# Performance work log

Measured on AMD Instinct MI355X. Metric: run time of the kernel, lower is better.

Reference implementation:

```python
import jax, jax.numpy as jnp
import numpy as np

B, N, D_IN, D_OUT = 4, 2048, 1024, 1024

def setup_inputs() -> dict:
    key = jax.random.key(0)
    ks = jax.random.split(key, 7)
    s_in = 1.0 / np.sqrt(D_IN)
    return {
        "X": jax.random.normal(ks[0], (B, N, D_IN), dtype=jnp.float32),
        "Wq": jax.random.uniform(ks[1], (D_IN, D_OUT), jnp.float32, -s_in, s_in),
        "bq": jax.random.uniform(ks[2], (D_OUT,), jnp.float32, -s_in, s_in),
        "Wk": jax.random.uniform(ks[3], (D_IN, D_OUT), jnp.float32, -s_in, s_in),
        "bk": jax.random.uniform(ks[4], (D_OUT,), jnp.float32, -s_in, s_in),
        "Wv": jax.random.uniform(ks[5], (D_IN, D_OUT), jnp.float32, -s_in, s_in),
        "bv": jax.random.uniform(ks[6], (D_OUT,), jnp.float32, -s_in, s_in),
    }

def reference(X, Wq, bq, Wk, bk, Wv, bv):
    # QKV projections: [B,N,D_in] @ [D_in,D_out] -> [B,N,D_out]
    q = jnp.einsum('bnd,de->bne', X, Wq) + bq
    k = jnp.einsum('bnd,de->bne', X, Wk) + bk
    v = jnp.einsum('bnd,de->bne', X, Wv) + bv
    # Unscaled attention (faithful: original has no 1/sqrt(d))
    scores = jnp.einsum('bne,bme->bnm', q, k)  # [B,N,N]
    weights = jax.nn.softmax(scores, axis=-1)
    return jnp.einsum('bnm,bme->bne', weights, v)
```

## Files before the change

kernel.cpp:

```cpp
#include <hip/hip_runtime.h>
#include <hip/hip_bf16.h>
#include <hip/hip_fp16.h>
#include <stdint.h>
#include <math.h>


typedef unsigned short ushort_t;
typedef __attribute__((ext_vector_type(8))) _Float16  f16x8;
typedef __attribute__((ext_vector_type(4))) _Float16  f16x4;
typedef __attribute__((ext_vector_type(4))) float     f32x4;

__device__ __forceinline__ void async_load16(const void* g, void* l) {
  __builtin_amdgcn_global_load_lds(
      (const __attribute__((address_space(1))) void*)g,
      (__attribute__((address_space(3))) void*)l, 16, 0, 0);
}

#define BARR do { __builtin_amdgcn_sched_barrier(0); \
                  __builtin_amdgcn_s_barrier();      \
                  __builtin_amdgcn_sched_barrier(0); } while (0)

#define NA0 0
#define NB0 16384
#define NA1 24576
#define NB1 40960

__device__ __forceinline__ void stage_A_n(const ushort_t* __restrict__ gb, long ldk,
                                          int k0, int q, ushort_t* lt, int t)
{
#pragma unroll
  for (int j = 0; j < 2; ++j) {
    const int i   = j * 64 + (t >> 3);
    const int row = ((i >> 5) << 6) | (q << 5) | (i & 31);
    const int ch  = (t & 7) ^ (row & 7);
    async_load16(gb + (long)row * ldk + k0 + ch * 8, lt + row * 64 + (t & 7) * 8);
  }
}

__device__ __forceinline__ void stage_B_n(const ushort_t* __restrict__ gb, long ldk,
                                          int k0, int q, ushort_t* lt, int t)
{
  const int i   = t >> 3;
  const int row = ((i >> 5) << 6) | (q << 5) | (i & 31);
  const int ch  = (t & 7) ^ (row & 7);
  async_load16(gb + (long)row * ldk + k0 + ch * 8, lt + row * 64 + (t & 7) * 8);
}

#define RD_A4(SET, BASE, QM)                                                  \
  do { _Pragma("unroll") for (int m_ = 0; m_ < 2; ++m_) {                     \
    SET[m_][0] = *(const f16x8*)&lds[(BASE) + (arow_l + (QM)*32 + m_*16) * 64 + ck0]; \
    SET[m_][1] = *(const f16x8*)&lds[(BASE) + (arow_l + (QM)*32 + m_*16) * 64 + ck1]; \
  } } while (0)

#define RD_B4(SET, BASE)                                                      \
  do { _Pragma("unroll") for (int q_ = 0; q_ < 2; ++q_)                       \
    _Pragma("unroll") for (int n_ = 0; n_ < 2; ++n_) {                        \
      SET[q_][n_][0] = *(const f16x8*)&lds[(BASE) + (brow_l + q_*32 + n_*16) * 64 + ck0]; \
      SET[q_][n_][1] = *(const f16x8*)&lds[(BASE) + (brow_l + q_*32 + n_*16) * 64 + ck1]; \
    } } while (0)

#define MM16(AS, BS, QM)                                                      \
  do { __builtin_amdgcn_s_setprio(1);                                         \
  _Pragma("unroll") for (int kh_ = 0; kh_ < 2; ++kh_)                         \
    _Pragma("unroll") for (int m_ = 0; m_ < 2; ++m_)                          \
      _Pragma("unroll") for (int n_ = 0; n_ < 2; ++n_) {                      \
        acc[(QM)*2+m_][n_]   = __builtin_amdgcn_mfma_f32_16x16x32_f16(        \
            AS[m_][kh_], BS[0][n_][kh_], acc[(QM)*2+m_][n_], 0, 0, 0);        \
        acc[(QM)*2+m_][2+n_] = __builtin_amdgcn_mfma_f32_16x16x32_f16(        \
            AS[m_][kh_], BS[1][n_][kh_], acc[(QM)*2+m_][2+n_], 0, 0, 0);      \
      }                                                                       \
  __builtin_amdgcn_s_setprio(0); } while (0)

#define MM16S(AS, BS, QM, SC)                                                 \
  do { __builtin_amdgcn_s_setprio(1);                                         \
  _Pragma("unroll") for (int m_ = 0; m_ < 2; ++m_)                            \
    _Pragma("unroll") for (int kh_ = 0; kh_ < 2; ++kh_) {                     \
      const f16x8 as_ = AS[m_][kh_] * (_Float16)(SC)[(QM)*2+m_];              \
      _Pragma("unroll") for (int n_ = 0; n_ < 2; ++n_) {                      \
        acc[(QM)*2+m_][n_]   = __builtin_amdgcn_mfma_f32_16x16x32_f16(        \
            as_, BS[0][n_][kh_], acc[(QM)*2+m_][n_], 0, 0, 0);                \
        acc[(QM)*2+m_][2+n_] = __builtin_amdgcn_mfma_f32_16x16x32_f16(        \
            as_, BS[1][n_][kh_], acc[(QM)*2+m_][2+n_], 0, 0, 0);              \
      } }                                                                     \
  __builtin_amdgcn_s_setprio(0); } while (0)

template<bool LAST>
__device__ __forceinline__ void iterRA(const ushort_t* __restrict__ Ab,
                                       const ushort_t* __restrict__ Bb,
                                       long lda, long ldb,
                                       ushort_t* lds, f32x4 (&acc)[4][4],
                                       int ka, int t, int arow_l, int brow_l,
                                       int ck0, int ck1,
                                       f16x8 (&aF)[2][2], f16x8 (&aG)[2][2],
                                       f16x8 (&bF)[2][2][2], f16x8 (&bG)[2][2][2])
{
  const int kc = ka + 128, kd = ka + 192;

  RD_A4(aG, NA0, 1);
  if constexpr (!LAST) { stage_A_n(Ab, lda, kc, 0, lds + NA0, t);
                         stage_B_n(Bb, ldb, kc, 0, lds + NB0, t); }
  BARR;
  MM16(aF, bF, 0);
  if constexpr (LAST) asm volatile("s_waitcnt vmcnt(0)" ::: "memory");
  else                asm volatile("s_waitcnt vmcnt(3)" ::: "memory");
  BARR;
  RD_A4(aF, NA1, 0);
  RD_B4(bG, NB1);
  if constexpr (!LAST) { stage_A_n(Ab, lda, kc, 1, lds + NA0, t);
                         stage_B_n(Bb, ldb, kc, 1, lds + NB0, t); }
  BARR;
  MM16(aG, bF, 1);
  BARR;
  RD_A4(aG, NA1, 1);
  if constexpr (!LAST) { stage_A_n(Ab, lda, kd, 0, lds + NA1, t);
                         stage_B_n(Bb, ldb, kd, 0, lds + NB1, t); }
  BARR;
  MM16(aF, bG, 0);
  if constexpr (!LAST) asm volatile("s_waitcnt vmcnt(3)" ::: "memory");
  BARR;
  if constexpr (!LAST) {
    RD_A4(aF, NA0, 0);
    RD_B4(bF, NB0);
    stage_A_n(Ab, lda, kd, 1, lds + NA1, t);
    stage_B_n(Bb, ldb, kd, 1, lds + NB1, t);
  }
  BARR;
  MM16(aG, bG, 1);
  BARR;
}

template<bool LAST>
__device__ __forceinline__ void pv_iterRA(const ushort_t* __restrict__ Ab,
                                          const ushort_t* __restrict__ Bb,
                                          ushort_t* lds, const float (*ScL)[256],
                                          f32x4 (&acc)[4][4],
                                          int ka, int t, int arow_l, int brow_l,
                                          int ck0, int ck1,
                                          f16x8 (&aF)[2][2], f16x8 (&aG)[2][2],
                                          f16x8 (&bF)[2][2][2], f16x8 (&bG)[2][2][2])
{
  const int kc = ka + 128, kd = ka + 192;
  const int cba = ka >> 6;
  float sa4[4], sb4[4];
#pragma unroll
  for (int s = 0; s < 4; ++s) {
    sa4[s] = ScL[cba][arow_l + s * 16];
    sb4[s] = ScL[cba + 1][arow_l + s * 16];
  }

  RD_A4(aG, NA0, 1);
  if constexpr (!LAST) { stage_A_n(Ab, 2048, kc, 0, lds + NA0, t);
                         stage_B_n(Bb, 2048, kc, 0, lds + NB0, t); }
  BARR;
  MM16S(aF, bF, 0, sa4);
  if constexpr (LAST) asm volatile("s_waitcnt vmcnt(0)" ::: "memory");
  else                asm volatile("s_waitcnt vmcnt(3)" ::: "memory");
  BARR;
  RD_A4(aF, NA1, 0);
  RD_B4(bG, NB1);
  if constexpr (!LAST) { stage_A_n(Ab, 2048, kc, 1, lds + NA0, t);
                         stage_B_n(Bb, 2048, kc, 1, lds + NB0, t); }
  BARR;
  MM16S(aG, bF, 1, sa4);
  BARR;
  RD_A4(aG, NA1, 1);
  if constexpr (!LAST) { stage_A_n(Ab, 2048, kd, 0, lds + NA1, t);
                         stage_B_n(Bb, 2048, kd, 0, lds + NB1, t); }
  BARR;
  MM16S(aF, bG, 0, sb4);
  if constexpr (!LAST) asm volatile("s_waitcnt vmcnt(3)" ::: "memory");
  BARR;
  if constexpr (!LAST) {
    RD_A4(aF, NA0, 0);
    RD_B4(bF, NB0);
    stage_A_n(Ab, 2048, kd, 1, lds + NA1, t);
    stage_B_n(Bb, 2048, kd, 1, lds + NB1, t);
  }
  BARR;
  MM16S(aG, bG, 1, sb4);
  BARR;
}

#define PROLOGUE_RA(LDA, LDB)                               \
  do {                                                      \
    stage_A_n(Ab, (LDA),  0, 0, lds + NA0, t);              \
    stage_B_n(Bb, (LDB),  0, 0, lds + NB0, t);              \
    stage_A_n(Ab, (LDA),  0, 1, lds + NA0, t);              \
    stage_B_n(Bb, (LDB),  0, 1, lds + NB0, t);              \
    asm volatile("s_waitcnt vmcnt(0)" ::: "memory");        \
    BARR;                                                   \
    RD_A4(aF, NA0, 0);                                      \
    RD_B4(bF, NB0);                                         \
    stage_A_n(Ab, (LDA), 64, 0, lds + NA1, t);              \
    stage_B_n(Bb, (LDB), 64, 0, lds + NB1, t);              \
    stage_A_n(Ab, (LDA), 64, 1, lds + NA1, t);              \
    stage_B_n(Bb, (LDB), 64, 1, lds + NB1, t);              \
    BARR;                                                   \
  } while (0)

__global__ __launch_bounds__(512, 2)
void qkv_ra_kernel(const ushort_t* __restrict__ A, const ushort_t* __restrict__ BT,
                   const float* __restrict__ bq, const float* __restrict__ bk,
                   const float* __restrict__ bvp,
                   __half* __restrict__ Qh, __half* __restrict__ Kh,
                   ushort_t* __restrict__ Vt)
{
  __shared__ __align__(16) ushort_t lds[49152];

  const int nb = gridDim.x * gridDim.y;
  int id = blockIdx.y * gridDim.x + blockIdx.x;
  id = (id & 7) * (nb >> 3) + (id >> 3);
  const int bx = id % gridDim.x;
  const int by = id / gridDim.x;

  const ushort_t* Ab = A  + (long)by * 256 * 1024;
  const ushort_t* Bb = BT + (long)bx * 128 * 1024;

  const int t    = threadIdx.x;
  const int lane = t & 63;
  const int wave = t >> 6;
  const int wr   = wave >> 1;
  const int wc   = wave & 1;
  const int arow_l = wr * 64 + (lane & 15);
  const int brow_l = wc * 64 + (lane & 15);
  const int ck0 = (((lane >> 4)    ) ^ (lane & 7)) * 8;
  const int ck1 = ((4 + (lane >> 4)) ^ (lane & 7)) * 8;

  f32x4 acc[4][4];
  const f32x4 zero = {0.0f, 0.0f, 0.0f, 0.0f};
#pragma unroll
  for (int i = 0; i < 4; ++i)
#pragma unroll
    for (int j = 0; j < 4; ++j) acc[i][j] = zero;

  f16x8 aF[2][2], aG[2][2], bF[2][2][2], bG[2][2][2];

  PROLOGUE_RA(1024, 1024);
#pragma unroll 1
  for (int it = 0; it < 7; ++it)
    iterRA<false>(Ab, Bb, 1024, 1024, lds, acc, it * 128, t, arow_l, brow_l,
                  ck0, ck1, aF, aG, bF, bG);
  iterRA<true>(Ab, Bb, 1024, 1024, lds, acc, 896, t, arow_l, brow_l,
               ck0, ck1, aF, aG, bF, bG);

  const int er = (lane >> 4) * 4, ec = lane & 15;
  const int tgt = bx >> 3;
  const float* bias = (tgt == 0) ? bq : (tgt == 1) ? bk : bvp;

#pragma unroll
  for (int ni = 0; ni < 4; ++ni) {
    const int col = (bx & 7) * 128 + wc * 64 + ni * 16 + ec;
    const float bval = bias[col];
#pragma unroll
    for (int mi = 0; mi < 4; ++mi) {
      const long grow0 = (long)by * 256 + wr * 64 + mi * 16 + er;
      if (tgt < 2) {
        __half* o = (tgt == 0) ? Qh : Kh;
#pragma unroll
        for (int r = 0; r < 4; ++r)
          o[(grow0 + r) * 1024 + col] = __float2half(acc[mi][ni][r] + bval);
      } else {
        const long b  = grow0 >> 11;
        const long ml = grow0 & 2047;
        f16x4 v4;
#pragma unroll
        for (int r = 0; r < 4; ++r) v4[r] = (_Float16)(acc[mi][ni][r] + bval);
        *(f16x4*)&Vt[b * 2097152 + (long)col * 2048 + ml] = v4;
      }
    }
  }
}

__global__ __launch_bounds__(512, 2)
void qk_ra_kernel(const ushort_t* __restrict__ Q, const ushort_t* __restrict__ Kh,
                  __half* __restrict__ S, float* __restrict__ PM, float* __restrict__ PS)
{
  __shared__ __align__(16) ushort_t lds[49152];

  const int nb = gridDim.x * gridDim.y;
  int id = blockIdx.y * gridDim.x + blockIdx.x;
  id = (id & 7) * (nb >> 3) + (id >> 3);
  const int bx = id % gridDim.x;
  const int by = id / gridDim.x;
  const long z = blockIdx.z;

  const ushort_t* Ab = Q  + z * 2048 * 1024 + (long)by * 256 * 1024;
  const ushort_t* Bb = Kh + z * 2048 * 1024 + (long)bx * 128 * 1024;
  __half* Sb = S + z * 2048 * 2048;

  const int t    = threadIdx.x;
  const int lane = t & 63;
  const int wave = t >> 6;
  const int wr   = wave >> 1;
  const int wc   = wave & 1;
  const int arow_l = wr * 64 + (lane & 15);
  const int brow_l = wc * 64 + (lane & 15);
  const int ck0 = (((lane >> 4)    ) ^ (lane & 7)) * 8;
  const int ck1 = ((4 + (lane >> 4)) ^ (lane & 7)) * 8;

  f32x4 acc[4][4];
  const f32x4 zero = {0.0f, 0.0f, 0.0f, 0.0f};
#pragma unroll
  for (int i = 0; i < 4; ++i)
#pragma unroll
    for (int j = 0; j < 4; ++j) acc[i][j] = zero;

  f16x8 aF[2][2], aG[2][2], bF[2][2][2], bG[2][2][2];

  PROLOGUE_RA(1024, 1024);
#pragma unroll 1
  for (int it = 0; it < 7; ++it)
    iterRA<false>(Ab, Bb, 1024, 1024, lds, acc, it * 128, t, arow_l, brow_l,
                  ck0, ck1, aF, aG, bF, bG);
  iterRA<true>(Ab, Bb, 1024, 1024, lds, acc, 896, t, arow_l, brow_l,
               ck0, ck1, aF, aG, bF, bG);

  const int er = (lane >> 4) * 4, ec = lane & 15;
  const int cc = bx * 2 + wc;
  float* PMb = PM + z * 32 * 2048 + (long)cc * 2048;
  float* PSb = PS + z * 32 * 2048 + (long)cc * 2048;

#pragma unroll
  for (int mi = 0; mi < 4; ++mi)
#pragma unroll
    for (int r = 0; r < 4; ++r) {
      float m = fmaxf(fmaxf(acc[mi][0][r], acc[mi][1][r]),
                      fmaxf(acc[mi][2][r], acc[mi][3][r]));
      m = fmaxf(m, __shfl_xor(m, 1));
      m = fmaxf(m, __shfl_xor(m, 2));
      m = fmaxf(m, __shfl_xor(m, 4));
      m = fmaxf(m, __shfl_xor(m, 8));
      float s = 0.0f;
#pragma unroll
      for (int ni = 0; ni < 4; ++ni) {
        const float e = __expf(acc[mi][ni][r] - m);
        acc[mi][ni][r] = e;
        s += e;
      }
      s += __shfl_xor(s, 1);
      s += __shfl_xor(s, 2);
      s += __shfl_xor(s, 4);
      s += __shfl_xor(s, 8);
      if (ec == 0) {
        const long row = (long)by * 256 + wr * 64 + mi * 16 + er + r;
        PMb[row] = m;
        PSb[row] = s;
      }
    }

#pragma unroll
  for (int ni = 0; ni < 4; ++ni) {
    const long col = (long)bx * 128 + wc * 64 + ni * 16 + ec;
#pragma unroll
    for (int mi = 0; mi < 4; ++mi)
#pragma unroll
      for (int r = 0; r < 4; ++r) {
        const long grow = (long)by * 256 + wr * 64 + mi * 16 + er + r;
        Sb[grow * 2048 + col] = __float2half(acc[mi][ni][r]);
      }
  }
}

__global__ __launch_bounds__(512, 2)
void pv_ra_kernel(const ushort_t* __restrict__ S, const ushort_t* __restrict__ Vt,
                  const float* __restrict__ PM, const float* __restrict__ PS,
                  float* __restrict__ Out)
{
  __shared__ __align__(16) ushort_t lds[49152];
  __shared__ float ScL[32][256];

  const int nb = gridDim.x * gridDim.y;
  int id = blockIdx.y * gridDim.x + blockIdx.x;
  id = (id & 7) * (nb >> 3) + (id >> 3);
  const int bx = id % gridDim.x;
  const int by = id / gridDim.x;
  const long z = blockIdx.z;

  const ushort_t* Ab = S  + z * 4194304 + (long)by * 256 * 2048;
  const ushort_t* Bb = Vt + z * 2097152 + (long)bx * 128 * 2048;
  float* Cb = Out + z * 2048 * 1024;

  const int t = threadIdx.x;

  if (t < 256) {
    const long row = (long)by * 256 + t;
    const float* PMb = PM + z * 32 * 2048;
    const float* PSb = PS + z * 32 * 2048;
    float pm[32];
    float m = -3.4e38f;
#pragma unroll
    for (int cb = 0; cb < 32; ++cb) {
      pm[cb] = PMb[(long)cb * 2048 + row];
      m = fmaxf(m, pm[cb]);
    }
    float l = 0.0f;
#pragma unroll
    for (int cb = 0; cb < 32; ++cb)
      l += PSb[(long)cb * 2048 + row] * __expf(pm[cb] - m);
    const float inv = 1.0f / l;
#pragma unroll
    for (int cb = 0; cb < 32; ++cb)
      ScL[cb][t] = __expf(pm[cb] - m) * inv;
  }
  __syncthreads();

  const int lane = t & 63;
  const int wave = t >> 6;
  const int wr   = wave >> 1;
  const int wc   = wave & 1;
  const int arow_l = wr * 64 + (lane & 15);
  const int brow_l = wc * 64 + (lane & 15);
  const int ck0 = (((lane >> 4)    ) ^ (lane & 7)) * 8;
  const int ck1 = ((4 + (lane >> 4)) ^ (lane & 7)) * 8;

  f32x4 acc[4][4];
  const f32x4 zero = {0.0f, 0.0f, 0.0f, 0.0f};
#pragma unroll
  for (int i = 0; i < 4; ++i)
#pragma unroll
    for (int j = 0; j < 4; ++j) acc[i][j] = zero;

  f16x8 aF[2][2], aG[2][2], bF[2][2][2], bG[2][2][2];

  PROLOGUE_RA(2048, 2048);
#pragma unroll 1
  for (int it = 0; it < 15; ++it)
    pv_iterRA<false>(Ab, Bb, lds, ScL, acc, it * 128, t, arow_l, brow_l,
                     ck0, ck1, aF, aG, bF, bG);
  pv_iterRA<true>(Ab, Bb, lds, ScL, acc, 1920, t, arow_l, brow_l,
                  ck0, ck1, aF, aG, bF, bG);

  const int er = (lane >> 4) * 4, ec = lane & 15;
#pragma unroll
  for (int ni = 0; ni < 4; ++ni) {
    const int gcol = bx * 128 + wc * 64 + ni * 16 + ec;
#pragma unroll
    for (int mi = 0; mi < 4; ++mi) {
#pragma unroll
      for (int r = 0; r < 4; ++r) {
        const long grow = (long)by * 256 + wr * 64 + mi * 16 + er + r;
        Cb[grow * 1024 + gcol] = acc[mi][ni][r];
      }
    }
  }
}

__global__ __launch_bounds__(256)
void prep_kernel(const float* __restrict__ W0, const float* __restrict__ W1,
                 const float* __restrict__ W2, __half* __restrict__ dstW,
                 const float* __restrict__ X, __half* __restrict__ Xh)
{
  __shared__ float tile[32][33];
  const int z = blockIdx.z;
  if (z < 3) {
    const float* src = (z == 0) ? W0 : (z == 1) ? W1 : W2;
    __half* d = dstW + (long)z * 1024 * 1024;
    const int c0 = blockIdx.x * 32;
    const int r0 = blockIdx.y * 32;
    const int tx = threadIdx.x & 31;
    const int ty = threadIdx.x >> 5;
#pragma unroll
    for (int i = 0; i < 32; i += 8)
      tile[ty + i][tx] = src[(long)(r0 + ty + i) * 1024 + (c0 + tx)];
    __syncthreads();
#pragma unroll
    for (int i = 0; i < 32; i += 8)
      d[(long)(c0 + ty + i) * 1024 + (r0 + tx)] = __float2half(tile[tx][ty + i]);
  } else {
    const int bid = blockIdx.y * gridDim.x + blockIdx.x;
    const long i = (((long)(z - 3) * 1024 + bid) * 256 + threadIdx.x) * 8;
    const float4 a = *(const float4*)(X + i);
    const float4 b = *(const float4*)(X + i + 4);
    f16x8 h;
    h[0] = (_Float16)a.x; h[1] = (_Float16)a.y; h[2] = (_Float16)a.z; h[3] = (_Float16)a.w;
    h[4] = (_Float16)b.x; h[5] = (_Float16)b.y; h[6] = (_Float16)b.z; h[7] = (_Float16)b.w;
    *(f16x8*)((ushort_t*)Xh + i) = h;
  }
}

__global__ __launch_bounds__(256)
void cvt_f32_f16_kernel(const float* __restrict__ src, __half* __restrict__ dst, long n)
{
  const long i = ((long)blockIdx.x * 256 + threadIdx.x) * 8;
  if (i + 8 > n) return;
  const float4 a = *(const float4*)(src + i);
  const float4 b = *(const float4*)(src + i + 4);
  f16x8 h;
  h[0] = (_Float16)a.x; h[1] = (_Float16)a.y; h[2] = (_Float16)a.z; h[3] = (_Float16)a.w;
  h[4] = (_Float16)b.x; h[5] = (_Float16)b.y; h[6] = (_Float16)b.z; h[7] = (_Float16)b.w;
  *(f16x8*)((ushort_t*)dst + i) = h;
}

__global__ __launch_bounds__(256)
void transpose_cvt3_kernel(const float* __restrict__ W0, const float* __restrict__ W1,
                           const float* __restrict__ W2, __half* __restrict__ dst)
{
  __shared__ float tile[32][33];
  const int z = blockIdx.z;
  const float* src = (z == 0) ? W0 : (z == 1) ? W1 : W2;
  __half* d = dst + (long)z * 1024 * 1024;
  const int c0 = blockIdx.x * 32;
  const int r0 = blockIdx.y * 32;
  const int tx = threadIdx.x & 31;
  const int ty = threadIdx.x >> 5;
#pragma unroll
  for (int i = 0; i < 32; i += 8)
    tile[ty + i][tx] = src[(long)(r0 + ty + i) * 1024 + (c0 + tx)];
  __syncthreads();
#pragma unroll
  for (int i = 0; i < 32; i += 8)
    d[(long)(c0 + ty + i) * 1024 + (r0 + tx)] = __float2half(tile[tx][ty + i]);
}

extern "C" void kernel_launch(void* const* d_in, const int* in_sizes, int n_in,
                              void* d_out, int out_size, void* d_ws, size_t ws_size,
                              hipStream_t stream)
{
  const int  Bb = 4, Nn = 2048, Dd = 1024;
  const long BN = (long)Bb * Nn;

  const float* X  = (const float*)d_in[0];
  const float* Wq = (const float*)d_in[1];
  const float* bq = (const float*)d_in[2];
  const float* Wk = (const float*)d_in[3];
  const float* bk = (const float*)d_in[4];
  const float* Wv = (const float*)d_in[5];
  const float* bv = (const float*)d_in[6];
  float* Out      = (float*)d_out;

  uint8_t* w = (uint8_t*)d_ws;
  ushort_t* Wt = (ushort_t*)w;  w += (size_t)3 * Dd * Dd * 2;

  const size_t statsBytes = (size_t)Bb * 32 * Nn * 4;
  const size_t fullNeed = (size_t)3 * Dd * Dd * 2
                        + 4 * ((size_t)BN * Dd * 2)
                        + (size_t)Bb * Nn * Nn * 2
                        + 2 * statsBytes;

  if (ws_size >= fullNeed) {
    ushort_t* Xh = (ushort_t*)w;  w += (size_t)BN * Dd * 2;
    ushort_t* Q  = (ushort_t*)w;  w += (size_t)BN * Dd * 2;
    ushort_t* Kb = (ushort_t*)w;  w += (size_t)BN * Dd * 2;
    ushort_t* Vt = (ushort_t*)w;  w += (size_t)BN * Dd * 2;
    ushort_t* S  = (ushort_t*)w;  w += (size_t)Bb * Nn * Nn * 2;
    float*    PM = (float*)w;     w += statsBytes;
    float*    PS = (float*)w;

    prep_kernel<<<dim3(32, 32, 7), 256, 0, stream>>>(Wq, Wk, Wv, (__half*)Wt, X, (__half*)Xh);

    qkv_ra_kernel<<<dim3(3 * Dd / 128, BN / 256, 1), 512, 0, stream>>>(
        Xh, Wt, bq, bk, bv, (__half*)Q, (__half*)Kb, Vt);

    qk_ra_kernel<<<dim3(Nn / 128, Nn / 256, Bb), 512, 0, stream>>>(
        Q, Kb, (__half*)S, PM, PS);

    pv_ra_kernel<<<dim3(Dd / 128, Nn / 256, Bb), 512, 0, stream>>>(
        S, Vt, PM, PS, Out);
  } else {
    ushort_t* Xh = (ushort_t*)w;  w += (size_t)Nn * Dd * 2;
    ushort_t* Q  = (ushort_t*)w;  w += (size_t)Nn * Dd * 2;
    ushort_t* Kb = (ushort_t*)w;  w += (size_t)Nn * Dd * 2;
    ushort_t* Vt = (ushort_t*)w;  w += (size_t)Nn * Dd * 2;
    ushort_t* S  = (ushort_t*)w;  w += (size_t)Nn * Nn * 2;
    float*    PM = (float*)w;     w += (size_t)32 * Nn * 4;
    float*    PS = (float*)w;

    transpose_cvt3_kernel<<<dim3(Dd / 32, Dd / 32, 3), 256, 0, stream>>>(Wq, Wk, Wv, (__half*)Wt);

    for (int b = 0; b < Bb; ++b) {
      const float* Xb = X + (long)b * Nn * Dd;
      cvt_f32_f16_kernel<<<dim3((unsigned)((long)Nn * Dd / (8 * 256))), 256, 0, stream>>>(
          Xb, (__half*)Xh, (long)Nn * Dd);
      qkv_ra_kernel<<<dim3(3 * Dd / 128, Nn / 256, 1), 512, 0, stream>>>(
          Xh, Wt, bq, bk, bv, (__half*)Q, (__half*)Kb, Vt);
      qk_ra_kernel<<<dim3(Nn / 128, Nn / 256, 1), 512, 0, stream>>>(
          Q, Kb, (__half*)S, PM, PS);
      pv_ra_kernel<<<dim3(Dd / 128, Nn / 256, 1), 512, 0, stream>>>(
          S, Vt, PM, PS, Out + (long)b * Nn * Dd);
    }
  }
}
```

Baseline: 245.3 us.

## Use 256x256 output tiles for Q/K projection and QK^T GEMMs

Adds a new GEMM pipeline (iterQ) with 256x256 block tiles, where each wave computes 128x64 with eight by four accumulators. The QK^T scores kernel and a new Q/K projection kernel use it, and the V projection (transposed output) moves to its own kernel with the old 256x128 tile. Larger tiles raise arithmetic intensity and cut global and LDS traffic per FLOP. In exchange they double accumulator registers and use 128KB of LDS per block, which may hurt occupancy, and the QK grid shrinks to 256 blocks. The fallback path is rewired to reuse prep_kernel.

```diff
diff --git a/kernel.cpp b/kernel.cpp
--- a/kernel.cpp
+++ b/kernel.cpp
@@ -20,13 +20,8 @@
                   __builtin_amdgcn_s_barrier();      \
                   __builtin_amdgcn_sched_barrier(0); } while (0)
 
-#define NA0 0
-#define NB0 16384
-#define NA1 24576
-#define NB1 40960
-
-__device__ __forceinline__ void stage_A_n(const ushort_t* __restrict__ gb, long ldk,
-                                          int k0, int q, ushort_t* lt, int t)
+__device__ __forceinline__ void stage_h256(const ushort_t* __restrict__ gb, long ldk,
+                                           int k0, int q, ushort_t* lt, int t)
 {
 #pragma unroll
   for (int j = 0; j < 2; ++j) {
@@ -37,14 +32,136 @@
   }
 }
 
-__device__ __forceinline__ void stage_B_n(const ushort_t* __restrict__ gb, long ldk,
-                                          int k0, int q, ushort_t* lt, int t)
+__device__ __forceinline__ void stage_h128(const ushort_t* __restrict__ gb, long ldk,
+                                           int k0, int q, ushort_t* lt, int t)
 {
   const int i   = t >> 3;
   const int row = ((i >> 5) << 6) | (q << 5) | (i & 31);
   const int ch  = (t & 7) ^ (row & 7);
   async_load16(gb + (long)row * ldk + k0 + ch * 8, lt + row * 64 + (t & 7) * 8);
 }
+
+#define QA0 0
+#define QB0 16384
+#define QA1 32768
+#define QB1 49152
+
+#define RD_AG(SET, BASE, G)                                                   \
+  do { _Pragma("unroll") for (int mi_ = 0; mi_ < 4; ++mi_) {                  \
+    const int r_ = arow_l + (2*(G) + (mi_ & 1) + 4*(mi_ >> 1)) * 16;          \
+    SET[mi_][0] = *(const f16x8*)&lds[(BASE) + r_ * 64 + ck0];                \
+    SET[mi_][1] = *(const f16x8*)&lds[(BASE) + r_ * 64 + ck1];                \
+  } } while (0)
+
+#define RD_BH(SET, BASE, H)                                                   \
+  do { _Pragma("unroll") for (int ni_ = 0; ni_ < 2; ++ni_) {                  \
+    const int r_ = brow_l + (2*(H) + ni_) * 16;                               \
+    SET[ni_][0] = *(const f16x8*)&lds[(BASE) + r_ * 64 + ck0];                \
+    SET[ni_][1] = *(const f16x8*)&lds[(BASE) + r_ * 64 + ck1];                \
+  } } while (0)
+
+#define MM16G(AS, BS, G, H)                                                   \
+  do { __builtin_amdgcn_s_setprio(1);                                         \
+  _Pragma("unroll") for (int kh_ = 0; kh_ < 2; ++kh_)                         \
+    _Pragma("unroll") for (int mi_ = 0; mi_ < 4; ++mi_)                       \
+      _Pragma("unroll") for (int ni_ = 0; ni_ < 2; ++ni_)                     \
+        acc[2*(G) + (mi_ & 1) + 4*(mi_ >> 1)][2*(H) + ni_] =                  \
+            __builtin_amdgcn_mfma_f32_16x16x32_f16(                           \
+                AS[mi_][kh_], BS[ni_][kh_],                                   \
+                acc[2*(G) + (mi_ & 1) + 4*(mi_ >> 1)][2*(H) + ni_], 0, 0, 0); \
+  __builtin_amdgcn_s_setprio(0); } while (0)
+
+template<bool LAST>
+__device__ __forceinline__ void iterQ(const ushort_t* __restrict__ Ab,
+                                      const ushort_t* __restrict__ Bb,
+                                      long lda, long ldb,
+                                      ushort_t* lds, f32x4 (&acc)[8][4],
+                                      int ka, int t, int arow_l, int brow_l,
+                                      int ck0, int ck1,
+                                      f16x8 (&aF)[4][2], f16x8 (&aG)[4][2],
+                                      f16x8 (&bF)[2][2], f16x8 (&bG)[2][2])
+{
+  const int kc = ka + 128, kd = ka + 192;
+
+  RD_BH(bG, QB0, 1);
+  if constexpr (!LAST) stage_h256(Bb, ldb, kc, 0, lds + QB0, t);
+  BARR; MM16G(aF, bF, 0, 0); BARR;
+
+  RD_AG(aG, QA0, 1);
+  if constexpr (!LAST) stage_h256(Bb, ldb, kc, 1, lds + QB0, t);
+  BARR; MM16G(aF, bG, 0, 1);
+  if constexpr (LAST) asm volatile("s_waitcnt vmcnt(2)" ::: "memory");
+  else                asm volatile("s_waitcnt vmcnt(6)" ::: "memory");
+  BARR;
+
+  RD_AG(aF, QA1, 0);
+  if constexpr (!LAST) stage_h256(Ab, lda, kc, 0, lds + QA0, t);
+  BARR; MM16G(aG, bG, 1, 1); BARR;
+
+  RD_BH(bG, QB1, 0);
+  if constexpr (!LAST) stage_h256(Ab, lda, kc, 1, lds + QA0, t);
+  BARR; MM16G(aG, bF, 1, 0); BARR;
+
+  RD_BH(bF, QB1, 1);
+  if constexpr (!LAST) stage_h256(Bb, ldb, kd, 0, lds + QB1, t);
+  BARR; MM16G(aF, bG, 0, 0);
+  if constexpr (LAST) asm volatile("s_waitcnt vmcnt(0)" ::: "memory");
+  else                asm volatile("s_waitcnt vmcnt(10)" ::: "memory");
+  BARR;
+
+  RD_AG(aG, QA1, 1);
+  if constexpr (!LAST) stage_h256(Bb, ldb, kd, 1, lds + QB1, t);
+  BARR; MM16G(aF, bF, 0, 1);
+  if constexpr (!LAST) asm volatile("s_waitcnt vmcnt(6)" ::: "memory");
+  BARR;
+
+  if constexpr (!LAST) {
+    RD_AG(aF, QA0, 0);
+    stage_h256(Ab, lda, kd, 0, lds + QA1, t);
+  }
+  BARR; MM16G(aG, bF, 1, 1); BARR;
+
+  if constexpr (!LAST) {
+    RD_BH(bF, QB0, 0);
+    stage_h256(Ab, lda, kd, 1, lds + QA1, t);
+  }
+  BARR; MM16G(aG, bG, 1, 0);
+  if constexpr (!LAST) asm volatile("s_waitcnt vmcnt(8)" ::: "memory");
+  BARR;
+}
+
+#define PROLOGUE_Q(LDA, LDB)                                \
+  do {                                                      \
+    stage_h256(Bb, (LDB),  0, 0, lds + QB0, t);             \
+    stage_h256(Bb, (LDB),  0, 1, lds + QB0, t);             \
+    stage_h256(Ab, (LDA),  0, 0, lds + QA0, t);             \
+    stage_h256(Ab, (LDA),  0, 1, lds + QA0, t);             \
+    stage_h256(Bb, (LDB), 64, 0, lds + QB1, t);             \
+    stage_h256(Bb, (LDB), 64, 1, lds + QB1, t);             \
+    stage_h256(Ab, (LDA), 64, 0, lds + QA1, t);             \
+    stage_h256(Ab, (LDA), 64, 1, lds + QA1, t);             \
+    asm volatile("s_waitcnt vmcnt(8)" ::: "memory");        \
+    BARR;                                                   \
+    RD_AG(aF, QA0, 0);                                      \
+    RD_BH(bF, QB0, 0);                                      \
+    BARR;                                                   \
+  } while (0)
+
+#define GEMM_Q(LDA, LDB)                                                      \
+  do {                                                                        \
+    PROLOGUE_Q(LDA, LDB);                                                     \
+    _Pragma("unroll 1")                                                       \
+    for (int it = 0; it < 7; ++it)                                            \
+      iterQ<false>(Ab, Bb, (LDA), (LDB), lds, acc, it * 128, t,               \
+                   arow_l, brow_l, ck0, ck1, aF, aG, bF, bG);                 \
+    iterQ<true>(Ab, Bb, (LDA), (LDB), lds, acc, 896, t,                       \
+                arow_l, brow_l, ck0, ck1, aF, aG, bF, bG);                    \
+  } while (0)
+
+#define NA0 0
+#define NB0 16384
+#define NA1 24576
+#define NB1 40960
 
 #define RD_A4(SET, BASE, QM)                                                  \
   do { _Pragma("unroll") for (int m_ = 0; m_ < 2; ++m_) {                     \
@@ -97,32 +214,35 @@
   const int kc = ka + 128, kd = ka + 192;
 
   RD_A4(aG, NA0, 1);
-  if constexpr (!LAST) { stage_A_n(Ab, lda, kc, 0, lds + NA0, t);
-                         stage_B_n(Bb, ldb, kc, 0, lds + NB0, t); }
+  if constexpr (!LAST) { stage_h256(Ab, lda, kc, 0, lds + NA0, t);
+                         stage_h128(Bb, ldb, kc, 0, lds + NB0, t); }
   BARR;
   MM16(aF, bF, 0);
   if constexpr (LAST) asm volatile("s_waitcnt vmcnt(0)" ::: "memory");
   else                asm volatile("s_waitcnt vmcnt(3)" ::: "memory");
   BARR;
+
   RD_A4(aF, NA1, 0);
   RD_B4(bG, NB1);
-  if constexpr (!LAST) { stage_A_n(Ab, lda, kc, 1, lds + NA0, t);
-                         stage_B_n(Bb, ldb, kc, 1, lds + NB0, t); }
+  if constexpr (!LAST) { stage_h256(Ab, lda, kc, 1, lds + NA0, t);
+                         stage_h128(Bb, ldb, kc, 1, lds + NB0, t); }
   BARR;
   MM16(aG, bF, 1);
   BARR;
+
   RD_A4(aG, NA1, 1);
-  if constexpr (!LAST) { stage_A_n(Ab, lda, kd, 0, lds + NA1, t);
-                         stage_B_n(Bb, ldb, kd, 0, lds + NB1, t); }
+  if constexpr (!LAST) { stage_h256(Ab, lda, kd, 0, lds + NA1, t);
+                         stage_h128(Bb, ldb, kd, 0, lds + NB1, t); }
   BARR;
   MM16(aF, bG, 0);
   if constexpr (!LAST) asm volatile("s_waitcnt vmcnt(3)" ::: "memory");
   BARR;
+
   if constexpr (!LAST) {
     RD_A4(aF, NA0, 0);
     RD_B4(bF, NB0);
-    stage_A_n(Ab, lda, kd, 1, lds + NA1, t);
-    stage_B_n(Bb, ldb, kd, 1, lds + NB1, t);
+    stage_h256(Ab, lda, kd, 1, lds + NA1, t);
+    stage_h128(Bb, ldb, kd, 1, lds + NB1, t);
   }
   BARR;
   MM16(aG, bG, 1);
@@ -149,32 +269,35 @@
   }
 
   RD_A4(aG, NA0, 1);
-  if constexpr (!LAST) { stage_A_n(Ab, 2048, kc, 0, lds + NA0, t);
-                         stage_B_n(Bb, 2048, kc, 0, lds + NB0, t); }
+  if constexpr (!LAST) { stage_h256(Ab, 2048, kc, 0, lds + NA0, t);
+                         stage_h128(Bb, 2048, kc, 0, lds + NB0, t); }
   BARR;
   MM16S(aF, bF, 0, sa4);
   if constexpr (LAST) asm volatile("s_waitcnt vmcnt(0)" ::: "memory");
   else                asm volatile("s_waitcnt vmcnt(3)" ::: "memory");
   BARR;
+
   RD_A4(aF, NA1, 0);
   RD_B4(bG, NB1);
-  if constexpr (!LAST) { stage_A_n(Ab, 2048, kc, 1, lds + NA0, t);
-                         stage_B_n(Bb, 2048, kc, 1, lds + NB0, t); }
+  if constexpr (!LAST) { stage_h256(Ab, 2048, kc, 1, lds + NA0, t);
+                         stage_h128(Bb, 2048, kc, 1, lds + NB0, t); }
   BARR;
   MM16S(aG, bF, 1, sa4);
   BARR;
+
   RD_A4(aG, NA1, 1);
-  if constexpr (!LAST) { stage_A_n(Ab, 2048, kd, 0, lds + NA1, t);
-                         stage_B_n(Bb, 2048, kd, 0, lds + NB1, t); }
+  if constexpr (!LAST) { stage_h256(Ab, 2048, kd, 0, lds + NA1, t);
+                         stage_h128(Bb, 2048, kd, 0, lds + NB1, t); }
   BARR;
   MM16S(aF, bG, 0, sb4);
   if constexpr (!LAST) asm volatile("s_waitcnt vmcnt(3)" ::: "memory");
   BARR;
+
   if constexpr (!LAST) {
     RD_A4(aF, NA0, 0);
     RD_B4(bF, NB0);
-    stage_A_n(Ab, 2048, kd, 1, lds + NA1, t);
-    stage_B_n(Bb, 2048, kd, 1, lds + NB1, t);
+    stage_h256(Ab, 2048, kd, 1, lds + NA1, t);
+    stage_h128(Bb, 2048, kd, 1, lds + NB1, t);
   }
   BARR;
   MM16S(aG, bG, 1, sb4);
@@ -183,29 +306,27 @@
 
 #define PROLOGUE_RA(LDA, LDB)                               \
   do {                                                      \
-    stage_A_n(Ab, (LDA),  0, 0, lds + NA0, t);              \
-    stage_B_n(Bb, (LDB),  0, 0, lds + NB0, t);              \
-    stage_A_n(Ab, (LDA),  0, 1, lds + NA0, t);              \
-    stage_B_n(Bb, (LDB),  0, 1, lds + NB0, t);              \
+    stage_h256(Ab, (LDA),  0, 0, lds + NA0, t);             \
+    stage_h128(Bb, (LDB),  0, 0, lds + NB0, t);             \
+    stage_h256(Ab, (LDA),  0, 1, lds + NA0, t);             \
+    stage_h128(Bb, (LDB),  0, 1, lds + NB0, t);             \
     asm volatile("s_waitcnt vmcnt(0)" ::: "memory");        \
     BARR;                                                   \
     RD_A4(aF, NA0, 0);                                      \
     RD_B4(bF, NB0);                                         \
-    stage_A_n(Ab, (LDA), 64, 0, lds + NA1, t);              \
-    stage_B_n(Bb, (LDB), 64, 0, lds + NB1, t);              \
-    stage_A_n(Ab, (LDA), 64, 1, lds + NA1, t);              \
-    stage_B_n(Bb, (LDB), 64, 1, lds + NB1, t);              \
+    stage_h256(Ab, (LDA), 64, 0, lds + NA1, t);             \
+    stage_h128(Bb, (LDB), 64, 0, lds + NB1, t);             \
+    stage_h256(Ab, (LDA), 64, 1, lds + NA1, t);             \
+    stage_h128(Bb, (LDB), 64, 1, lds + NB1, t);             \
     BARR;                                                   \
   } while (0)
 
 __global__ __launch_bounds__(512, 2)
-void qkv_ra_kernel(const ushort_t* __restrict__ A, const ushort_t* __restrict__ BT,
+void qkproj_kernel(const ushort_t* __restrict__ A, const ushort_t* __restrict__ BT,
                    const float* __restrict__ bq, const float* __restrict__ bk,
-                   const float* __restrict__ bvp,
-                   __half* __restrict__ Qh, __half* __restrict__ Kh,
-                   ushort_t* __restrict__ Vt)
-{
-  __shared__ __align__(16) ushort_t lds[49152];
+                   __half* __restrict__ Qh, __half* __restrict__ Kh)
+{
+  __shared__ __align__(16) ushort_t lds[65536];
 
   const int nb = gridDim.x * gridDim.y;
   int id = blockIdx.y * gridDim.x + blockIdx.x;
@@ -214,7 +335,62 @@
   const int by = id / gridDim.x;
 
   const ushort_t* Ab = A  + (long)by * 256 * 1024;
-  const ushort_t* Bb = BT + (long)bx * 128 * 1024;
+  const ushort_t* Bb = BT + (long)bx * 256 * 1024;
+
+  const int t    = threadIdx.x;
+  const int lane = t & 63;
+  const int wave = t >> 6;
+  const int wr   = wave >> 2;
+  const int wc   = wave & 3;
+  const int arow_l = wr * 128 + (lane & 15);
+  const int brow_l = wc * 64  + (lane & 15);
+  const int ck0 = (((lane >> 4)    ) ^ (lane & 7)) * 8;
+  const int ck1 = ((4 + (lane >> 4)) ^ (lane & 7)) * 8;
+
+  f32x4 acc[8][4];
+  const f32x4 zero = {0.0f, 0.0f, 0.0f, 0.0f};
+#pragma unroll
+  for (int i = 0; i < 8; ++i)
+#pragma unroll
+    for (int j = 0; j < 4; ++j) acc[i][j] = zero;
+
+  f16x8 aF[4][2], aG[4][2], bF[2][2], bG[2][2];
+
+  GEMM_Q(1024, 1024);
+
+  const int er = (lane >> 4) * 4, ec = lane & 15;
+  const int tgt = bx >> 2;
+  const float* bias = (tgt == 0) ? bq : bk;
+  __half* o = (tgt == 0) ? Qh : Kh;
+
+#pragma unroll
+  for (int ni = 0; ni < 4; ++ni) {
+    const int col = (bx & 3) * 256 + wc * 64 + ni * 16 + ec;
+    const float bval = bias[col];
+#pragma unroll
+    for (int mi = 0; mi < 8; ++mi) {
+      const long grow0 = (long)by * 256 + wr * 128 + mi * 16 + er;
+#pragma unroll
+      for (int r = 0; r < 4; ++r)
+        o[(grow0 + r) * 1024 + col] = __float2half(acc[mi][ni][r] + bval);
+    }
+  }
+}
+
+__global__ __launch_bounds__(512, 2)
+void vproj_kernel(const ushort_t* __restrict__ A, const ushort_t* __restrict__ BT,
+                  const float* __restrict__ bvp, ushort_t* __restrict__ Vt)
+{
+  __shared__ __align__(16) ushort_t lds[49152];
+
+  const int nb = gridDim.x * gridDim.y;
+  int id = blockIdx.y * gridDim.x + blockIdx.x;
+  id = (id & 7) * (nb >> 3) + (id >> 3);
+  const int bx = id % gridDim.x;
+  const int by = id / gridDim.x;
+
+  const ushort_t* Ab = A  + (long)by * 256 * 1024;
+  const ushort_t* Bb = BT + (long)(16 + bx) * 128 * 1024;
 
   const int t    = threadIdx.x;
   const int lane = t & 63;
@@ -244,38 +420,28 @@
                ck0, ck1, aF, aG, bF, bG);
 
   const int er = (lane >> 4) * 4, ec = lane & 15;
-  const int tgt = bx >> 3;
-  const float* bias = (tgt == 0) ? bq : (tgt == 1) ? bk : bvp;
-
 #pragma unroll
   for (int ni = 0; ni < 4; ++ni) {
-    const int col = (bx & 7) * 128 + wc * 64 + ni * 16 + ec;
-    const float bval = bias[col];
+    const int col = bx * 128 + wc * 64 + ni * 16 + ec;
+    const float bval = bvp[col];
 #pragma unroll
     for (int mi = 0; mi < 4; ++mi) {
       const long grow0 = (long)by * 256 + wr * 64 + mi * 16 + er;
-      if (tgt < 2) {
-        __half* o = (tgt == 0) ? Qh : Kh;
-#pragma unroll
-        for (int r = 0; r < 4; ++r)
-          o[(grow0 + r) * 1024 + col] = __float2half(acc[mi][ni][r] + bval);
-      } else {
-        const long b  = grow0 >> 11;
-        const long ml = grow0 & 2047;
-        f16x4 v4;
-#pragma unroll
-        for (int r = 0; r < 4; ++r) v4[r] = (_Float16)(acc[mi][ni][r] + bval);
-        *(f16x4*)&Vt[b * 2097152 + (long)col * 2048 + ml] = v4;
-      }
+      const long b  = grow0 >> 11;
+      const long ml = grow0 & 2047;
+      f16x4 v4;
+#pragma unroll
+      for (int r = 0; r < 4; ++r) v4[r] = (_Float16)(acc[mi][ni][r] + bval);
+      *(f16x4*)&Vt[b * 2097152 + (long)col * 2048 + ml] = v4;
     }
   }
 }
 
 __global__ __launch_bounds__(512, 2)
-void qk_ra_kernel(const ushort_t* __restrict__ Q, const ushort_t* __restrict__ Kh,
-                  __half* __restrict__ S, float* __restrict__ PM, float* __restrict__ PS)
-{
-  __shared__ __align__(16) ushort_t lds[49152];
+void qkattn_kernel(const ushort_t* __restrict__ Q, const ushort_t* __restrict__ Kh,
+                   __half* __restrict__ S, float* __restrict__ PM, float* __restrict__ PS)
+{
+  __shared__ __align__(16) ushort_t lds[65536];
 
   const int nb = gridDim.x * gridDim.y;
   int id = blockIdx.y * gridDim.x + blockIdx.x;
@@ -285,43 +451,37 @@
   const long z = blockIdx.z;
 
   const ushort_t* Ab = Q  + z * 2048 * 1024 + (long)by * 256 * 1024;
-  const ushort_t* Bb = Kh + z * 2048 * 1024 + (long)bx * 128 * 1024;
+  const ushort_t* Bb = Kh + z * 2048 * 1024 + (long)bx * 256 * 1024;
   __half* Sb = S + z * 2048 * 2048;
 
   const int t    = threadIdx.x;
   const int lane = t & 63;
   const int wave = t >> 6;
-  const int wr   = wave >> 1;
-  const int wc   = wave & 1;
-  const int arow_l = wr * 64 + (lane & 15);
-  const int brow_l = wc * 64 + (lane & 15);
+  const int wr   = wave >> 2;
+  const int wc   = wave & 3;
+  const int arow_l = wr * 128 + (lane & 15);
+  const int brow_l = wc * 64  + (lane & 15);
   const int ck0 = (((lane >> 4)    ) ^ (lane & 7)) * 8;
   const int ck1 = ((4 + (lane >> 4)) ^ (lane & 7)) * 8;
 
-  f32x4 acc[4][4];
+  f32x4 acc[8][4];
   const f32x4 zero = {0.0f, 0.0f, 0.0f, 0.0f};
 #pragma unroll
-  for (int i = 0; i < 4; ++i)
+  for (int i = 0; i < 8; ++i)
 #pragma unroll
     for (int j = 0; j < 4; ++j) acc[i][j] = zero;
 
-  f16x8 aF[2][2], aG[2][2], bF[2][2][2], bG[2][2][2];
-
-  PROLOGUE_RA(1024, 1024);
-#pragma unroll 1
-  for (int it = 0; it < 7; ++it)
-    iterRA<false>(Ab, Bb, 1024, 1024, lds, acc, it * 128, t, arow_l, brow_l,
-                  ck0, ck1, aF, aG, bF, bG);
-  iterRA<true>(Ab, Bb, 1024, 1024, lds, acc, 896, t, arow_l, brow_l,
-               ck0, ck1, aF, aG, bF, bG);
+  f16x8 aF[4][2], aG[4][2], bF[2][2], bG[2][2];
+
+  GEMM_Q(1024, 1024);
 
   const int er = (lane >> 4) * 4, ec = lane & 15;
-  const int cc = bx * 2 + wc;
+  const int cc = bx * 4 + wc;
   float* PMb = PM + z * 32 * 2048 + (long)cc * 2048;
   float* PSb = PS + z * 32 * 2048 + (long)cc * 2048;
 
 #pragma unroll
-  for (int mi = 0; mi < 4; ++mi)
+  for (int mi = 0; mi < 8; ++mi)
 #pragma unroll
     for (int r = 0; r < 4; ++r) {
       float m = fmaxf(fmaxf(acc[mi][0][r], acc[mi][1][r]),
@@ -342,7 +502,7 @@
       s += __shfl_xor(s, 4);
       s += __shfl_xor(s, 8);
       if (ec == 0) {
-        const long row = (long)by * 256 + wr * 64 + mi * 16 + er + r;
+        const long row = (long)by * 256 + wr * 128 + mi * 16 + er + r;
         PMb[row] = m;
         PSb[row] = s;
       }
@@ -350,12 +510,12 @@
 
 #pragma unroll
   for (int ni = 0; ni < 4; ++ni) {
-    const long col = (long)bx * 128 + wc * 64 + ni * 16 + ec;
-#pragma unroll
-    for (int mi = 0; mi < 4; ++mi)
+    const long col = (long)bx * 256 + wc * 64 + ni * 16 + ec;
+#pragma unroll
+    for (int mi = 0; mi < 8; ++mi)
 #pragma unroll
       for (int r = 0; r < 4; ++r) {
-        const long grow = (long)by * 256 + wr * 64 + mi * 16 + er + r;
+        const long grow = (long)by * 256 + wr * 128 + mi * 16 + er + r;
         Sb[grow * 2048 + col] = __float2half(acc[mi][ni][r]);
       }
   }
@@ -478,40 +638,6 @@
   }
 }
 
-__global__ __launch_bounds__(256)
-void cvt_f32_f16_kernel(const float* __restrict__ src, __half* __restrict__ dst, long n)
-{
-  const long i = ((long)blockIdx.x * 256 + threadIdx.x) * 8;
-  if (i + 8 > n) return;
-  const float4 a = *(const float4*)(src + i);
-  const float4 b = *(const float4*)(src + i + 4);
-  f16x8 h;
-  h[0] = (_Float16)a.x; h[1] = (_Float16)a.y; h[2] = (_Float16)a.z; h[3] = (_Float16)a.w;
-  h[4] = (_Float16)b.x; h[5] = (_Float16)b.y; h[6] = (_Float16)b.z; h[7] = (_Float16)b.w;
-  *(f16x8*)((ushort_t*)dst + i) = h;
-}
-
-__global__ __launch_bounds__(256)
-void transpose_cvt3_kernel(const float* __restrict__ W0, const float* __restrict__ W1,
-                           const float* __restrict__ W2, __half* __restrict__ dst)
-{
-  __shared__ float tile[32][33];
-  const int z = blockIdx.z;
-  const float* src = (z == 0) ? W0 : (z == 1) ? W1 : W2;
-  __half* d = dst + (long)z * 1024 * 1024;
-  const int c0 = blockIdx.x * 32;
-  const int r0 = blockIdx.y * 32;
-  const int tx = threadIdx.x & 31;
-  const int ty = threadIdx.x >> 5;
-#pragma unroll
-  for (int i = 0; i < 32; i += 8)
-    tile[ty + i][tx] = src[(long)(r0 + ty + i) * 1024 + (c0 + tx)];
-  __syncthreads();
-#pragma unroll
-  for (int i = 0; i < 32; i += 8)
-    d[(long)(c0 + ty + i) * 1024 + (r0 + tx)] = __float2half(tile[tx][ty + i]);
-}
-
 extern "C" void kernel_launch(void* const* d_in, const int* in_sizes, int n_in,
                               void* d_out, int out_size, void* d_ws, size_t ws_size,
                               hipStream_t stream)
@@ -548,10 +674,12 @@
 
     prep_kernel<<<dim3(32, 32, 7), 256, 0, stream>>>(Wq, Wk, Wv, (__half*)Wt, X, (__half*)Xh);
 
-    qkv_ra_kernel<<<dim3(3 * Dd / 128, BN / 256, 1), 512, 0, stream>>>(
-        Xh, Wt, bq, bk, bv, (__half*)Q, (__half*)Kb, Vt);
-
-    qk_ra_kernel<<<dim3(Nn / 128, Nn / 256, Bb), 512, 0, stream>>>(
+    qkproj_kernel<<<dim3(8, BN / 256, 1), 512, 0, stream>>>(
+        Xh, Wt, bq, bk, (__half*)Q, (__half*)Kb);
+
+    vproj_kernel<<<dim3(8, BN / 256, 1), 512, 0, stream>>>(Xh, Wt, bv, Vt);
+
+    qkattn_kernel<<<dim3(Nn / 256, Nn / 256, Bb), 512, 0, stream>>>(
         Q, Kb, (__half*)S, PM, PS);
 
     pv_ra_kernel<<<dim3(Dd / 128, Nn / 256, Bb), 512, 0, stream>>>(
@@ -565,15 +693,14 @@
     float*    PM = (float*)w;     w += (size_t)32 * Nn * 4;
     float*    PS = (float*)w;
 
-    transpose_cvt3_kernel<<<dim3(Dd / 32, Dd / 32, 3), 256, 0, stream>>>(Wq, Wk, Wv, (__half*)Wt);
-
     for (int b = 0; b < Bb; ++b) {
       const float* Xb = X + (long)b * Nn * Dd;
-      cvt_f32_f16_kernel<<<dim3((unsigned)((long)Nn * Dd / (8 * 256))), 256, 0, stream>>>(
-          Xb, (__half*)Xh, (long)Nn * Dd);
-      qkv_ra_kernel<<<dim3(3 * Dd / 128, Nn / 256, 1), 512, 0, stream>>>(
-          Xh, Wt, bq, bk, bv, (__half*)Q, (__half*)Kb, Vt);
-      qk_ra_kernel<<<dim3(Nn / 128, Nn / 256, 1), 512, 0, stream>>>(
+      prep_kernel<<<dim3(32, 32, b == 0 ? 4 : 1), 256, 0, stream>>>(
+          Wq, Wk, Wv, (__half*)Wt, Xb, (__half*)Xh);
+      qkproj_kernel<<<dim3(8, Nn / 256, 1), 512, 0, stream>>>(
+          Xh, Wt, bq, bk, (__half*)Q, (__half*)Kb);
+      vproj_kernel<<<dim3(8, Nn / 256, 1), 512, 0, stream>>>(Xh, Wt, bv, Vt);
+      qkattn_kernel<<<dim3(Nn / 256, Nn / 256, 1), 512, 0, stream>>>(
           Q, Kb, (__half*)S, PM, PS);
       pv_ra_kernel<<<dim3(Dd / 128, Nn / 256, 1), 512, 0, stream>>>(
           S, Vt, PM, PS, Out + (long)b * Nn * Dd);
```

Result: slower. 384.2 us (+56.6%).
